# Kernel optimization log

Hardware: AMD Instinct MI355X
Metric: run time of the kernel (lower is better)

Reference implementation:

```python
import jax, jax.numpy as jnp
import numpy as np
import math

EPS = 1e-6
D_MODEL = 512
N_HEADS = 8
D_K = D_MODEL // N_HEADS
B = 8192
K = 32
M = 16


def setup_inputs() -> dict:
    key = jax.random.key(0)
    ks = jax.random.split(key, 9)
    s = 1.0 / math.sqrt(D_MODEL)
    return {
        "x_anc": jax.random.normal(ks[0], (B, D_MODEL), dtype=jnp.float32),
        "x_nei": jax.random.normal(ks[1], (B, K, D_MODEL), dtype=jnp.float32),
        "pi": jax.random.uniform(ks[2], (B, N_HEADS, M), dtype=jnp.float32),
        "tau": jax.random.uniform(ks[3], (N_HEADS,), dtype=jnp.float32),
        "ew": jax.random.uniform(ks[4], (B, K, M), dtype=jnp.float32),
        "W_q": jax.random.normal(ks[5], (D_MODEL, D_MODEL), dtype=jnp.float32) * s,
        "W_k": jax.random.normal(ks[6], (D_MODEL, D_MODEL), dtype=jnp.float32) * s,
        "W_v": jax.random.normal(ks[7], (D_MODEL, D_MODEL), dtype=jnp.float32) * s,
        "W_o": jax.random.normal(ks[8], (D_MODEL, D_MODEL), dtype=jnp.float32) * s,
    }


def reference(x_anc, x_nei, pi, tau, ew, W_q, W_k, W_v, W_o):
    b, k, _ = x_nei.shape
    h, dk = N_HEADS, D_K
    # Projections (bias-free linears)
    Q = (x_anc @ W_q).reshape(b, h, dk)            # [B,H,dk]
    K_ = (x_nei @ W_k).reshape(b, k, h, dk)        # [B,K,H,dk]
    V_ = (x_nei @ W_v).reshape(b, k, h, dk)        # [B,K,H,dk]
    # Geometry-routed log bias
    A_eff = jnp.einsum("bhm,bkm->bhk", pi, ew)     # [B,H,K]
    graph_bias = jnp.log(tau[None, :, None] * A_eff + EPS)
    # Attention over K neighbors
    scores = jnp.einsum("bhd,bkhd->bhk", Q, K_) / math.sqrt(dk)
    attn = jax.nn.softmax(scores + graph_bias, axis=-1)  # dropout is identity (eval)
    out = jnp.einsum("bhk,bkhd->bhd", attn, V_).reshape(b, h * dk)
    return out @ W_o
```

## Files before the change

### kernel.cpp

```cpp
#include <hip/hip_runtime.h>
#include <hip/hip_bf16.h>
#include <hip/hip_fp16.h>


typedef _Float16 f16;
typedef __attribute__((ext_vector_type(8))) _Float16 f16x8;
typedef __attribute__((ext_vector_type(4))) float f32x4;
typedef unsigned int u32;
typedef unsigned short u16;

#define MFMA16(a, b, c) __builtin_amdgcn_mfma_f32_16x16x32_f16(a, b, c, 0, 0, 0)

__device__ __forceinline__ u32 pk2(float x, float y) {
    f16 a = (f16)x, b = (f16)y;
    u16 ua = __builtin_bit_cast(u16, a), ub = __builtin_bit_cast(u16, b);
    return (u32)ua | ((u32)ub << 16);
}

__global__ void cvt_f16(const float* __restrict__ s, f16* __restrict__ d, int n8) {
    int i = blockIdx.x * blockDim.x + threadIdx.x;
    if (i < n8) {
        float4 a = ((const float4*)s)[i * 2];
        float4 b = ((const float4*)s)[i * 2 + 1];
        f16x8 v;
        v[0] = (f16)a.x; v[1] = (f16)a.y; v[2] = (f16)a.z; v[3] = (f16)a.w;
        v[4] = (f16)b.x; v[5] = (f16)b.y; v[6] = (f16)b.z; v[7] = (f16)b.w;
        ((f16x8*)d)[i] = v;
    }
}

__global__ void transpose_w_f16(const float* __restrict__ wq, const float* __restrict__ wv,
                                const float* __restrict__ wo, f16* __restrict__ dq,
                                f16* __restrict__ dv, f16* __restrict__ dmo) {
    int z = blockIdx.z;
    const float* s = (z == 0) ? wq : ((z == 1) ? wv : wo);
    f16* d = (z == 0) ? dq : ((z == 1) ? dv : dmo);
    int t = threadIdx.x;
    int j = blockIdx.x * 64 + (t & 63);
    int c0 = blockIdx.y * 32 + (t >> 6) * 8;
    f16x8 v;
#pragma unroll
    for (int i = 0; i < 8; i++) v[i] = (f16)s[(size_t)(c0 + i) * 512 + j];
    *(f16x8*)&d[(size_t)j * 512 + c0] = v;
}

#define LDSROW 40
template <bool OUTF32>
__global__ __launch_bounds__(256) void gemm16(
    const f16* __restrict__ A, int lda, int aColZ,
    const f16* __restrict__ Bt, int ldb, int btRowZ, int btColZ,
    void* __restrict__ Cv, int ldc, int cColZ,
    int Ktot, int Nvalid) {
    __shared__ __align__(16) f16 aL[128 * LDSROW];
    __shared__ __align__(16) f16 bL[128 * LDSROW];
    int z = blockIdx.z;
    const f16* Ab = A + (size_t)blockIdx.x * 128 * lda + (size_t)z * aColZ;
    const f16* Bb = Bt + ((size_t)blockIdx.y * 128 + (size_t)z * btRowZ) * ldb + (size_t)z * btColZ;
    int t = threadIdx.x, l = t & 63, wid = t >> 6;
    int g = l >> 4, l15 = l & 15;
    int wr = wid >> 1, wc = wid & 1;
    int nclamp = Nvalid - blockIdx.y * 128 - 1;
    f32x4 acc[4][4] = {};
    int sr0 = wid * 32 + (l >> 2);
    int sr1 = sr0 + 16;
    int ch = (l & 3) * 8;
    for (int k0 = 0; k0 < Ktot; k0 += 32) {
        __syncthreads();
        f16x8 a0 = *(const f16x8*)(Ab + (size_t)sr0 * lda + k0 + ch);
        f16x8 a1 = *(const f16x8*)(Ab + (size_t)sr1 * lda + k0 + ch);
        int br0 = sr0 <= nclamp ? sr0 : nclamp;
        int br1 = sr1 <= nclamp ? sr1 : nclamp;
        f16x8 b0 = *(const f16x8*)(Bb + (size_t)br0 * ldb + k0 + ch);
        f16x8 b1 = *(const f16x8*)(Bb + (size_t)br1 * ldb + k0 + ch);
        *(f16x8*)&aL[sr0 * LDSROW + ch] = a0;
        *(f16x8*)&aL[sr1 * LDSROW + ch] = a1;
        *(f16x8*)&bL[sr0 * LDSROW + ch] = b0;
        *(f16x8*)&bL[sr1 * LDSROW + ch] = b1;
        __syncthreads();
        f16x8 af[4], bf[4];
#pragma unroll
        for (int m = 0; m < 4; m++) af[m] = *(f16x8*)&aL[(wr * 64 + m * 16 + l15) * LDSROW + g * 8];
#pragma unroll
        for (int n = 0; n < 4; n++) bf[n] = *(f16x8*)&bL[(wc * 64 + n * 16 + l15) * LDSROW + g * 8];
#pragma unroll
        for (int m = 0; m < 4; m++)
#pragma unroll
            for (int n = 0; n < 4; n++)
                acc[m][n] = MFMA16(af[m], bf[n], acc[m][n]);
    }
    size_t row0 = (size_t)blockIdx.x * 128 + wr * 64;
#pragma unroll
    for (int m = 0; m < 4; m++) {
#pragma unroll
        for (int n = 0; n < 4; n++) {
            int cl = blockIdx.y * 128 + wc * 64 + n * 16 + l15;
            if (cl < Nvalid) {
#pragma unroll
                for (int r = 0; r < 4; r++) {
                    size_t off = (row0 + m * 16 + g * 4 + r) * (size_t)ldc + (size_t)z * cColZ + cl;
                    if constexpr (OUTF32) ((float*)Cv)[off] = acc[m][n][r];
                    else ((f16*)Cv)[off] = (f16)acc[m][n][r];
                }
            }
        }
    }
}

__global__ __launch_bounds__(64) void attn_core(
    const float* __restrict__ xn,
    const float* __restrict__ pi,
    const float* __restrict__ tau,
    const float* __restrict__ ew,
    const f16* Qt,
    f16* mixed)
{
    __shared__ __align__(16) f16 xs[32 * 512];
    __shared__ __align__(16) f16 pis[16 * 32];
    __shared__ __align__(16) f16 ews[32 * 32];
    __shared__ __align__(16) f16 attns[16 * 32];
    __shared__ float taus[8];
    int b = blockIdx.x;
    int l = threadIdx.x, g = l >> 4, l15 = l & 15;

    u32* pz = (u32*)pis;
    for (int i = l; i < 256; i += 64) pz[i] = 0;
    u32* ez = (u32*)ews;
    for (int i = l; i < 512; i += 64) ez[i] = 0;
    if (l < 8) taus[l] = tau[l];
    __syncthreads();
    {
        float2 v = ((const float2*)(pi + (size_t)b * 128))[l];
        ((u32*)pis)[(l >> 3) * 16 + (l & 7)] = pk2(v.x, v.y);
    }
    {
        const float2* e2 = (const float2*)(ew + (size_t)b * 512);
        int k = l >> 1, hh = l & 1;
#pragma unroll
        for (int j = 0; j < 4; j++) {
            float2 v = e2[k * 8 + hh * 4 + j];
            ((u32*)ews)[k * 16 + hh * 4 + j] = pk2(v.x, v.y);
        }
    }
    {
        const float4* src = (const float4*)(xn + (size_t)b * 16384);
#pragma unroll 8
        for (int i = 0; i < 64; i++) {
            int idx = i * 64 + l;
            float4 v = src[idx];
            int k = idx >> 7, c0 = (idx & 127) << 2;
            uint2 u;
            u.x = pk2(v.x, v.y);
            u.y = pk2(v.z, v.w);
            int e = ((c0 >> 4) << 9) | ((k >> 2) << 6) | ((k & 3) << 4) | (c0 & 15);
            *(uint2*)&xs[e] = u;
        }
    }
    __syncthreads();

    f32x4 zz = {};
    f16x8 pa = *(f16x8*)&pis[l15 * 32 + g * 8];
    f16x8 ebf0 = *(f16x8*)&ews[l15 * 32 + g * 8];
    f16x8 ebf1 = *(f16x8*)&ews[(16 + l15) * 32 + g * 8];
    f32x4 ae0 = MFMA16(pa, ebf0, zz);
    f32x4 ae1 = MFMA16(pa, ebf1, zz);
    float bias0[4], bias1[4];
#pragma unroll
    for (int r = 0; r < 4; r++) {
        if (g < 2) {
            float tv = taus[4 * g + r];
            bias0[r] = __logf(tv * ae0[r] + 1e-6f);
            bias1[r] = __logf(tv * ae1[r] + 1e-6f);
        } else {
            bias0[r] = 0.f;
            bias1[r] = 0.f;
        }
    }

    f32x4 sc0 = {}, sc1 = {};
    const f16* qb = Qt + (size_t)b * 4096 + (size_t)(l15 < 8 ? l15 : 7) * 512 + g * 8;
#pragma unroll
    for (int kk = 0; kk < 16; kk++) {
        f16x8 a = *(const f16x8*)(qb + kk * 32);
        if (l15 >= 8) {
#pragma unroll
            for (int j = 0; j < 8; j++) a[j] = (f16)0.f;
        }
        int e0 = ((kk * 2 + (g >> 1)) << 9) | ((l15 >> 2) << 6) | ((l15 & 3) << 4) | ((g & 1) << 3);
        f16x8 b0 = *(f16x8*)&xs[e0];
        f16x8 b1 = *(f16x8*)&xs[e0 + 256];
        sc0 = MFMA16(a, b0, sc0);
        sc1 = MFMA16(a, b1, sc1);
    }

#pragma unroll
    for (int r = 0; r < 4; r++) {
        float x0 = sc0[r] * 0.125f + bias0[r];
        float x1 = sc1[r] * 0.125f + bias1[r];
        float m = fmaxf(x0, x1);
        m = fmaxf(m, __shfl_xor(m, 1, 64));
        m = fmaxf(m, __shfl_xor(m, 2, 64));
        m = fmaxf(m, __shfl_xor(m, 4, 64));
        m = fmaxf(m, __shfl_xor(m, 8, 64));
        float e0 = __expf(x0 - m), e1 = __expf(x1 - m);
        float s = e0 + e1;
        s += __shfl_xor(s, 1, 64);
        s += __shfl_xor(s, 2, 64);
        s += __shfl_xor(s, 4, 64);
        s += __shfl_xor(s, 8, 64);
        float inv = 1.0f / s;
        float a0 = e0 * inv, a1 = e1 * inv;
        if (g >= 2) { a0 = 0.f; a1 = 0.f; }
        attns[(4 * g + r) * 32 + l15] = (f16)a0;
        attns[(4 * g + r) * 32 + 16 + l15] = (f16)a1;
    }
    __syncthreads();

    f16x8 af = *(f16x8*)&attns[l15 * 32 + g * 8];
    size_t ob = (size_t)b * 4096;
#pragma unroll 4
    for (int nt = 0; nt < 32; nt++) {
        f16x8 bf;
        int base = nt * 512 + l15 + g * 128;
#pragma unroll
        for (int s = 0; s < 8; s++) bf[s] = xs[base + (s >> 2) * 64 + (s & 3) * 16];
        f32x4 d = MFMA16(af, bf, zz);
        if (g < 2) {
#pragma unroll
            for (int r = 0; r < 4; r++)
                mixed[ob + (size_t)(4 * g + r) * 512 + nt * 16 + l15] = (f16)d[r];
        }
    }
}

extern "C" void kernel_launch(void* const* d_in, const int* in_sizes, int n_in,
                              void* d_out, int out_size, void* d_ws, size_t ws_size,
                              hipStream_t stream) {
    const float* x_anc = (const float*)d_in[0];
    const float* x_nei = (const float*)d_in[1];
    const float* pi    = (const float*)d_in[2];
    const float* tau   = (const float*)d_in[3];
    const float* ew    = (const float*)d_in[4];
    const float* W_q   = (const float*)d_in[5];
    const float* W_k   = (const float*)d_in[6];
    const float* W_v   = (const float*)d_in[7];
    const float* W_o   = (const float*)d_in[8];
    float* out = (float*)d_out;

    char* w = (char*)d_ws;
    f16* Qt = (f16*)w;          w += 67108864 + 16384;
    f16* xanc16 = (f16*)w;
    f16* Vh = (f16*)w;          w += 8388608;
    f16* Q16 = (f16*)w;         w += 8388608;
    f16* wqT = (f16*)w;         w += 524288;
    f16* wk16 = (f16*)w;        w += 524288;
    f16* wvT = (f16*)w;         w += 524288;
    f16* woT = (f16*)w;         w += 524288;

    cvt_f16<<<2048, 256, 0, stream>>>(x_anc, xanc16, 524288);
    cvt_f16<<<128, 256, 0, stream>>>(W_k, wk16, 32768);
    transpose_w_f16<<<dim3(8, 16, 3), 256, 0, stream>>>(W_q, W_v, W_o, wqT, wvT, woT);

    gemm16<false><<<dim3(64, 4, 1), 256, 0, stream>>>(xanc16, 512, 0, wqT, 512, 0, 0,
                                                      Q16, 512, 0, 512, 512);
    gemm16<false><<<dim3(64, 4, 8), 256, 0, stream>>>(Q16, 512, 64, wk16, 512, 0, 64,
                                                      Qt, 4096, 512, 64, 512);
    attn_core<<<8192, 64, 0, stream>>>(x_nei, pi, tau, ew, Qt, Qt);

    gemm16<false><<<dim3(64, 1, 8), 256, 0, stream>>>(Qt, 4096, 512, wvT, 512, 64, 0,
                                                      Vh, 512, 64, 512, 64);
    gemm16<true><<<dim3(64, 4, 1), 256, 0, stream>>>(Vh, 512, 0, woT, 512, 0, 0,
                                                     out, 512, 0, 512, 512);
}
```

Measured before the change: 835.7 us.

## Use four waves per attention block and prefetch Q before x_nei staging

The attention kernel now runs 256 threads per batch row instead of 64. The x_nei fp32 load and fp16 conversion is split across all four waves, and the weighted-sum output tiles are split too, eight tiles per wave. Wave 0 loads its Q fragments into registers while waves 1 and 2 load pi and ew, which overlaps the Q global latency with staging. The score and softmax phase now runs only on wave 0 while the other waves wait at a barrier, and the larger block may lower occupancy through LDS and register use.

New measurement: 812.3 us. 2.8% less time.

```diff
diff --git a/kernel.cpp b/kernel.cpp
--- a/kernel.cpp
+++ b/kernel.cpp
@@ -106,7 +106,7 @@
     }
 }
 
-__global__ __launch_bounds__(64) void attn_core(
+__global__ __launch_bounds__(256) void attn_core(
     const float* __restrict__ xn,
     const float* __restrict__ pi,
     const float* __restrict__ tau,
@@ -120,19 +120,30 @@
     __shared__ __align__(16) f16 attns[16 * 32];
     __shared__ float taus[8];
     int b = blockIdx.x;
-    int l = threadIdx.x, g = l >> 4, l15 = l & 15;
-
-    u32* pz = (u32*)pis;
-    for (int i = l; i < 256; i += 64) pz[i] = 0;
-    u32* ez = (u32*)ews;
-    for (int i = l; i < 512; i += 64) ez[i] = 0;
-    if (l < 8) taus[l] = tau[l];
+    int t = threadIdx.x;
+    int w = t >> 6, l = t & 63, g = l >> 4, l15 = l & 15;
+
+    ((u32*)pis)[t] = 0;
+    ((u32*)ews)[t] = 0;
+    ((u32*)ews)[t + 256] = 0;
+    if (t < 8) taus[t] = tau[t];
     __syncthreads();
-    {
+
+    f16x8 qreg[16];
+    if (w == 0) {
+        const f16* qb = Qt + (size_t)b * 4096 + (size_t)l15 * 512 + g * 8;
+#pragma unroll
+        for (int kk = 0; kk < 16; kk++) {
+            f16x8 qv;
+#pragma unroll
+            for (int j = 0; j < 8; j++) qv[j] = (f16)0.f;
+            if (l15 < 8) qv = *(const f16x8*)(qb + kk * 32);
+            qreg[kk] = qv;
+        }
+    } else if (w == 1) {
         float2 v = ((const float2*)(pi + (size_t)b * 128))[l];
         ((u32*)pis)[(l >> 3) * 16 + (l & 7)] = pk2(v.x, v.y);
-    }
-    {
+    } else if (w == 2) {
         const float2* e2 = (const float2*)(ew + (size_t)b * 512);
         int k = l >> 1, hh = l & 1;
 #pragma unroll
@@ -143,9 +154,9 @@
     }
     {
         const float4* src = (const float4*)(xn + (size_t)b * 16384);
-#pragma unroll 8
-        for (int i = 0; i < 64; i++) {
-            int idx = i * 64 + l;
+#pragma unroll
+        for (int i = 0; i < 16; i++) {
+            int idx = i * 256 + t;
             float4 v = src[idx];
             int k = idx >> 7, c0 = (idx & 127) << 2;
             uint2 u;
@@ -158,67 +169,64 @@
     __syncthreads();
 
     f32x4 zz = {};
-    f16x8 pa = *(f16x8*)&pis[l15 * 32 + g * 8];
-    f16x8 ebf0 = *(f16x8*)&ews[l15 * 32 + g * 8];
-    f16x8 ebf1 = *(f16x8*)&ews[(16 + l15) * 32 + g * 8];
-    f32x4 ae0 = MFMA16(pa, ebf0, zz);
-    f32x4 ae1 = MFMA16(pa, ebf1, zz);
-    float bias0[4], bias1[4];
-#pragma unroll
-    for (int r = 0; r < 4; r++) {
-        if (g < 2) {
-            float tv = taus[4 * g + r];
-            bias0[r] = __logf(tv * ae0[r] + 1e-6f);
-            bias1[r] = __logf(tv * ae1[r] + 1e-6f);
-        } else {
-            bias0[r] = 0.f;
-            bias1[r] = 0.f;
-        }
-    }
-
-    f32x4 sc0 = {}, sc1 = {};
-    const f16* qb = Qt + (size_t)b * 4096 + (size_t)(l15 < 8 ? l15 : 7) * 512 + g * 8;
-#pragma unroll
-    for (int kk = 0; kk < 16; kk++) {
-        f16x8 a = *(const f16x8*)(qb + kk * 32);
-        if (l15 >= 8) {
-#pragma unroll
-            for (int j = 0; j < 8; j++) a[j] = (f16)0.f;
-        }
-        int e0 = ((kk * 2 + (g >> 1)) << 9) | ((l15 >> 2) << 6) | ((l15 & 3) << 4) | ((g & 1) << 3);
-        f16x8 b0 = *(f16x8*)&xs[e0];
-        f16x8 b1 = *(f16x8*)&xs[e0 + 256];
-        sc0 = MFMA16(a, b0, sc0);
-        sc1 = MFMA16(a, b1, sc1);
-    }
-
-#pragma unroll
-    for (int r = 0; r < 4; r++) {
-        float x0 = sc0[r] * 0.125f + bias0[r];
-        float x1 = sc1[r] * 0.125f + bias1[r];
-        float m = fmaxf(x0, x1);
-        m = fmaxf(m, __shfl_xor(m, 1, 64));
-        m = fmaxf(m, __shfl_xor(m, 2, 64));
-        m = fmaxf(m, __shfl_xor(m, 4, 64));
-        m = fmaxf(m, __shfl_xor(m, 8, 64));
-        float e0 = __expf(x0 - m), e1 = __expf(x1 - m);
-        float s = e0 + e1;
-        s += __shfl_xor(s, 1, 64);
-        s += __shfl_xor(s, 2, 64);
-        s += __shfl_xor(s, 4, 64);
-        s += __shfl_xor(s, 8, 64);
-        float inv = 1.0f / s;
-        float a0 = e0 * inv, a1 = e1 * inv;
-        if (g >= 2) { a0 = 0.f; a1 = 0.f; }
-        attns[(4 * g + r) * 32 + l15] = (f16)a0;
-        attns[(4 * g + r) * 32 + 16 + l15] = (f16)a1;
+    if (w == 0) {
+        f16x8 pa = *(f16x8*)&pis[l15 * 32 + g * 8];
+        f16x8 ebf0 = *(f16x8*)&ews[l15 * 32 + g * 8];
+        f16x8 ebf1 = *(f16x8*)&ews[(16 + l15) * 32 + g * 8];
+        f32x4 ae0 = MFMA16(pa, ebf0, zz);
+        f32x4 ae1 = MFMA16(pa, ebf1, zz);
+        float bias0[4], bias1[4];
+#pragma unroll
+        for (int r = 0; r < 4; r++) {
+            if (g < 2) {
+                float tv = taus[4 * g + r];
+                bias0[r] = __logf(tv * ae0[r] + 1e-6f);
+                bias1[r] = __logf(tv * ae1[r] + 1e-6f);
+            } else {
+                bias0[r] = 0.f;
+                bias1[r] = 0.f;
+            }
+        }
+
+        f32x4 sc0 = {}, sc1 = {};
+#pragma unroll
+        for (int kk = 0; kk < 16; kk++) {
+            int e0 = ((kk * 2 + (g >> 1)) << 9) | ((l15 >> 2) << 6) | ((l15 & 3) << 4) | ((g & 1) << 3);
+            f16x8 b0 = *(f16x8*)&xs[e0];
+            f16x8 b1 = *(f16x8*)&xs[e0 + 256];
+            sc0 = MFMA16(qreg[kk], b0, sc0);
+            sc1 = MFMA16(qreg[kk], b1, sc1);
+        }
+
+#pragma unroll
+        for (int r = 0; r < 4; r++) {
+            float x0 = sc0[r] * 0.125f + bias0[r];
+            float x1 = sc1[r] * 0.125f + bias1[r];
+            float m = fmaxf(x0, x1);
+            m = fmaxf(m, __shfl_xor(m, 1, 64));
+            m = fmaxf(m, __shfl_xor(m, 2, 64));
+            m = fmaxf(m, __shfl_xor(m, 4, 64));
+            m = fmaxf(m, __shfl_xor(m, 8, 64));
+            float e0 = __expf(x0 - m), e1 = __expf(x1 - m);
+            float s = e0 + e1;
+            s += __shfl_xor(s, 1, 64);
+            s += __shfl_xor(s, 2, 64);
+            s += __shfl_xor(s, 4, 64);
+            s += __shfl_xor(s, 8, 64);
+            float inv = 1.0f / s;
+            float a0 = e0 * inv, a1 = e1 * inv;
+            if (g >= 2) { a0 = 0.f; a1 = 0.f; }
+            attns[(4 * g + r) * 32 + l15] = (f16)a0;
+            attns[(4 * g + r) * 32 + 16 + l15] = (f16)a1;
+        }
     }
     __syncthreads();
 
     f16x8 af = *(f16x8*)&attns[l15 * 32 + g * 8];
     size_t ob = (size_t)b * 4096;
-#pragma unroll 4
-    for (int nt = 0; nt < 32; nt++) {
+#pragma unroll
+    for (int j = 0; j < 8; j++) {
+        int nt = w * 8 + j;
         f16x8 bf;
         int base = nt * 512 + l15 + g * 128;
 #pragma unroll
@@ -264,7 +272,7 @@
                                                       Q16, 512, 0, 512, 512);
     gemm16<false><<<dim3(64, 4, 8), 256, 0, stream>>>(Q16, 512, 64, wk16, 512, 0, 64,
                                                       Qt, 4096, 512, 64, 512);
-    attn_core<<<8192, 64, 0, stream>>>(x_nei, pi, tau, ew, Qt, Qt);
+    attn_core<<<8192, 256, 0, stream>>>(x_nei, pi, tau, ew, Qt, Qt);
 
     gemm16<false><<<dim3(64, 1, 8), 256, 0, stream>>>(Qt, 4096, 512, wvT, 512, 64, 0,
                                                       Vh, 512, 64, 512, 64);
```
